# Kernel tuning notes

Measured on AMD Instinct MI355X. Metric: run time of the kernel, lower is better.

## Reference

```python
import jax, jax.numpy as jnp
import numpy as np

B, S, E, H, W, HID, V, OUT, L = 2, 2048, 512, 8, 5, 2048, 32000, 6, 6
DH = E // H
SCALE = DH ** -0.5
PAD = (W - 1) // 2
SK = S - W + 1  # number of k/v windows from torch unfold


def setup_inputs() -> dict:
    key = jax.random.key(0)
    ks = jax.random.split(key, 16)
    def g(i, shape, s):
        return jax.random.normal(ks[i], shape, jnp.float32) * s
    return {
        "inputs": jax.random.randint(ks[0], (B, S), 0, V),
        "emb": g(1, (V, E), 0.02),
        "ln_w": jnp.ones((E,), jnp.float32),
        "ln_b": jnp.zeros((E,), jnp.float32),
        "q_w": g(2, (E, E), E ** -0.5), "q_b": jnp.zeros((E,), jnp.float32),
        "k_w": g(3, (E, E), E ** -0.5), "k_b": jnp.zeros((E,), jnp.float32),
        "v_w": g(4, (E, E), E ** -0.5), "v_b": jnp.zeros((E,), jnp.float32),
        "fc1_w": g(5, (E, HID), E ** -0.5), "fc1_b": jnp.zeros((HID,), jnp.float32),
        "fc2_w": g(6, (HID, E), HID ** -0.5), "fc2_b": jnp.zeros((E,), jnp.float32),
        "out_w": g(7, (E * S, OUT), (E * S) ** -0.5), "out_b": jnp.zeros((OUT,), jnp.float32),
    }


def _pos_encoding():
    pos = jnp.arange(S, dtype=jnp.float32)[:, None]
    div = jnp.exp(jnp.arange(0, E, 2, dtype=jnp.float32) * (-np.log(10000.0) / E))
    pe = jnp.zeros((S, E), jnp.float32)
    pe = pe.at[:, 0::2].set(jnp.sin(pos * div)).at[:, 1::2].set(jnp.cos(pos * div))
    return pe


def reference(inputs, emb, ln_w, ln_b, q_w, q_b, k_w, k_b, v_w, v_b,
              fc1_w, fc1_b, fc2_w, fc2_b, out_w, out_b):
    x = emb[inputs] + _pos_encoding()  # [B,S,E]

    def ln(t):
        m = t.mean(-1, keepdims=True)
        v_ = t.var(-1, keepdims=True)
        return (t - m) / jnp.sqrt(v_ + 1e-5) * ln_w + ln_b

    def attn(x):
        def heads(w, b):
            return (x @ w + b).reshape(B, S, H, DH).transpose(0, 2, 1, 3)  # [B,H,S,dh]
        q, k, v = heads(q_w, q_b), heads(k_w, k_b), heads(v_w, v_b)
        qp = jnp.pad(q, ((0, 0), (0, 0), (PAD, PAD), (0, 0)))  # [B,H,S+W-1,dh]
        # torch unfold -> windows [..., dh, W]; einsum contracts dh AND W, so flatten both.
        q_un = jnp.stack([qp[:, :, j:j + S, :] for j in range(W)], axis=-1).reshape(B, H, S, DH * W)
        k_un = jnp.stack([k[:, :, j:j + SK, :] for j in range(W)], axis=-1).reshape(B, H, SK, DH * W)
        scores = jnp.einsum('bhqf,bhkf->bhqk', q_un, k_un) * SCALE  # [B,H,S,SK]
        a = jax.nn.softmax(scores, axis=-1)
        # output einsum 'bnqk,bnkdh->bnqd' sums attn-weighted v over k AND window dim;
        # since attn is independent of window pos, presum v over the window.
        v_sum = sum(v[:, :, j:j + SK, :] for j in range(W))  # [B,H,SK,dh]
        o = jnp.einsum('bhqk,bhkd->bhqd', a, v_sum)
        return o.transpose(0, 2, 1, 3).reshape(B, S, E)

    for _ in range(L):
        x = ln(attn(x))
        x = (jax.nn.relu(x @ fc1_w + fc1_b) @ fc2_w + fc2_b) + x
        x = ln(x)
    return x.reshape(B, -1) @ out_w + out_b  # [B,OUT]
```

## Files before the change

### kernel.cpp

```cpp
#include <hip/hip_runtime.h>
#include <math.h>


namespace {
constexpr int kB   = 2;
constexpr int kS   = 2048;
constexpr int kE   = 512;
constexpr int kH   = 8;
constexpr int kDH  = 64;
constexpr int kSK  = 2044;
constexpr int kHID = 2048;
constexpr int kL   = 6;
constexpr float kScaleL2 = 0.125f * 1.44269504088896f;
constexpr int kTok = kB * kS;
constexpr int kNX  = kTok * kE;
constexpr int kQKV = 3 * kE;
constexpr int kSQ  = 72;
constexpr int kSV  = 136;
}

using f16x8   = __attribute__((ext_vector_type(8))) _Float16;
using floatx4 = __attribute__((ext_vector_type(4))) float;
using uint2v  = __attribute__((ext_vector_type(2))) unsigned int;
using uint4v  = __attribute__((ext_vector_type(4))) unsigned int;

static __device__ __forceinline__ unsigned short f2h(float f) {
  return __builtin_bit_cast(unsigned short, (_Float16)f);
}
static __device__ __forceinline__ float h2f(unsigned short u) {
  return (float)__builtin_bit_cast(_Float16, u);
}
static __device__ __forceinline__ unsigned int pk2h(float a, float b) {
  return __builtin_bit_cast(unsigned int, __builtin_amdgcn_cvt_pkrtz(a, b));
}
static __device__ __forceinline__ void gload_lds16(const unsigned short* g,
                                                   unsigned short* l) {
  __builtin_amdgcn_global_load_lds(
      (const __attribute__((address_space(1))) void*)g,
      (__attribute__((address_space(3))) void*)l, 16, 0, 0);
}
static __device__ __forceinline__ float red16(float x, bool hi) {
  const unsigned u = __builtin_bit_cast(unsigned, x);
  const uint2v r = __builtin_amdgcn_permlane16_swap(u, u, false, false);
  return __builtin_bit_cast(float, hi ? r[0] : r[1]);
}
static __device__ __forceinline__ float red32(float x, bool hi) {
  const unsigned u = __builtin_bit_cast(unsigned, x);
  const uint2v r = __builtin_amdgcn_permlane32_swap(u, u, false, false);
  return __builtin_bit_cast(float, hi ? r[0] : r[1]);
}

__global__ __launch_bounds__(256) void embed_kernel(const int* __restrict__ idx,
        const float* __restrict__ emb, unsigned short* __restrict__ X) {
  const int bs  = blockIdx.x;
  const int s   = bs & (kS - 1);
  const int tok = idx[bs];
  const int t   = threadIdx.x;
#pragma unroll
  for (int r = 0; r < 2; ++r) {
    const int e = t + 256 * r;
    const int i = e >> 1;
    const float dv  = __expf((float)(2 * i) * (-9.210340371976184f / (float)kE));
    const float ang = (float)s * dv;
    const float pe  = (e & 1) ? cosf(ang) : sinf(ang);
    X[bs * kE + e] = f2h(emb[tok * kE + e] + pe);
  }
}

__global__ __launch_bounds__(256) void tcast_kernel(const float* __restrict__ src,
        unsigned short* __restrict__ dst, int K, int N) {
  __shared__ float t[32][33];
  const int tid = threadIdx.x;
  const int tx = tid & 31, ty = tid >> 5;
  const int n0 = blockIdx.x * 32, k0 = blockIdx.y * 32;
#pragma unroll
  for (int p = 0; p < 4; ++p)
    t[ty + 8 * p][tx] = src[(size_t)(k0 + ty + 8 * p) * N + n0 + tx];
  __syncthreads();
#pragma unroll
  for (int p = 0; p < 4; ++p)
    dst[(size_t)(n0 + ty + 8 * p) * K + k0 + tx] = f2h(t[tx][ty + 8 * p]);
}

__global__ __launch_bounds__(256) void qkvb_kernel(const float* __restrict__ qb,
        const float* __restrict__ kb, const float* __restrict__ vb,
        float* __restrict__ dst) {
  const int i = blockIdx.x * 256 + threadIdx.x;
  dst[i] = (i < 512) ? qb[i] : ((i < 1024) ? kb[i - 512] : vb[i - 1024]);
}

template <int RELU, int RES>
__global__ __launch_bounds__(256) void mfma_gemm(const unsigned short* __restrict__ A,
        const unsigned short* __restrict__ Bt, const float* __restrict__ bias,
        const unsigned short* __restrict__ Rm, unsigned short* __restrict__ C,
        int M, int N, int K) {
  __shared__ __align__(16) unsigned short As[2][128 * 32];
  __shared__ __align__(16) unsigned short Bs[2][128 * 32];
  const int tid = threadIdx.x;
  const int m0 = blockIdx.y * 128, n0 = blockIdx.x * 128;
  const int wid = tid >> 6, lane = tid & 63;
  const int lm = lane & 15, quad = lane >> 4;
  const int wm = (wid & 1) * 64, wn = (wid >> 1) * 64;
  const int bn = tid >> 2, bk = (tid & 3) * 8;
  const int wslot = wid * 512;
#pragma unroll
  for (int p = 0; p < 2; ++p) {
    gload_lds16(&A[(size_t)(m0 + bn + 64 * p) * K + bk], &As[0][wslot + p * 2048]);
    gload_lds16(&Bt[(size_t)(n0 + bn + 64 * p) * K + bk], &Bs[0][wslot + p * 2048]);
  }
  __syncthreads();
  floatx4 acc[4][4] = {};
  for (int k0 = 0; k0 < K; k0 += 32) {
    const int cur = (k0 >> 5) & 1;
    const int kn = k0 + 32;
    if (kn < K) {
#pragma unroll
      for (int p = 0; p < 2; ++p) {
        gload_lds16(&A[(size_t)(m0 + bn + 64 * p) * K + kn + bk],
                    &As[cur ^ 1][wslot + p * 2048]);
        gload_lds16(&Bt[(size_t)(n0 + bn + 64 * p) * K + kn + bk],
                    &Bs[cur ^ 1][wslot + p * 2048]);
      }
    }
    f16x8 af[4], bf[4];
#pragma unroll
    for (int t = 0; t < 4; ++t) {
      af[t] = *(const f16x8*)&As[cur][(wm + t * 16 + lm) * 32 + quad * 8];
      bf[t] = *(const f16x8*)&Bs[cur][(wn + t * 16 + lm) * 32 + quad * 8];
    }
#pragma unroll
    for (int mt = 0; mt < 4; ++mt)
#pragma unroll
      for (int nt = 0; nt < 4; ++nt)
        acc[mt][nt] = __builtin_amdgcn_mfma_f32_16x16x32_f16(
            af[mt], bf[nt], acc[mt][nt], 0, 0, 0);
    __syncthreads();
  }
#pragma unroll
  for (int mt = 0; mt < 4; ++mt) {
#pragma unroll
    for (int nt = 0; nt < 4; ++nt) {
      const int n = n0 + wn + nt * 16 + lm;
      const float bv = bias[n];
#pragma unroll
      for (int r = 0; r < 4; ++r) {
        const int m = m0 + wm + mt * 16 + quad * 4 + r;
        float o = acc[mt][nt][r] + bv;
        if (RES) o += h2f(Rm[(size_t)m * N + n]);
        if (RELU) o = fmaxf(o, 0.f);
        C[(size_t)m * N + n] = f2h(o);
      }
    }
  }
}

__global__ __launch_bounds__(256) void vsumt_kernel(const unsigned short* __restrict__ QKVh,
        unsigned short* __restrict__ VsT) {
  const int t0 = blockIdx.x * 64;
  const int h = blockIdx.y, b = blockIdx.z;
  const int tid = threadIdx.x;
  __shared__ float Ls[68 * 65];
  for (int id = tid; id < 68 * 8; id += 256) {
    const int row = id >> 3, d8 = (id & 7) * 8;
    const int gt = t0 + row;
    float v[8];
    if (gt < kS) {
      const unsigned short* p =
          &QKVh[(size_t)(b * kS + gt) * kQKV + 2 * kE + h * kDH + d8];
      const ushort4 a = *(const ushort4*)p;
      const ushort4 c = *(const ushort4*)(p + 4);
      v[0] = h2f(a.x); v[1] = h2f(a.y); v[2] = h2f(a.z); v[3] = h2f(a.w);
      v[4] = h2f(c.x); v[5] = h2f(c.y); v[6] = h2f(c.z); v[7] = h2f(c.w);
    } else {
#pragma unroll
      for (int j = 0; j < 8; ++j) v[j] = 0.f;
    }
#pragma unroll
    for (int j = 0; j < 8; ++j) Ls[row * 65 + d8 + j] = v[j];
  }
  __syncthreads();
  const int t4 = (tid & 15) * 4;
#pragma unroll
  for (int c = 0; c < 4; ++c) {
    const int d = (tid >> 4) + 16 * c;
    ushort4 o;
    unsigned short* op = (unsigned short*)&o;
#pragma unroll
    for (int j = 0; j < 4; ++j) {
      const int tl = t4 + j;
      float s = Ls[(tl + 0) * 65 + d] + Ls[(tl + 1) * 65 + d]
              + Ls[(tl + 2) * 65 + d] + Ls[(tl + 3) * 65 + d]
              + Ls[(tl + 4) * 65 + d];
      if (t0 + tl >= kSK) s = 0.f;
      op[j] = f2h(s);
    }
    *(ushort4*)&VsT[((size_t)(b * kH + h) * kDH + d) * (size_t)kS + t0 + t4] = o;
  }
}

__global__ __launch_bounds__(512) void flash_kernel(const unsigned short* __restrict__ QKVh,
        const unsigned short* __restrict__ VsT, unsigned short* __restrict__ O) {
  const int tid = threadIdx.x;
  const int qt = blockIdx.x, h = blockIdx.y, b = blockIdx.z;
  const int q0 = qt * 64;
  const int wid = tid >> 6, lane = tid & 63;
  const int lm = lane & 15, quad = lane >> 4;
  const bool h16 = (lane & 16) != 0, h32 = (lane & 32) != 0;
  const int wq = wid >> 2, wt = wid & 3;
  const int bh = b * kH + h;

  __shared__ __align__(16) unsigned short Qs[68 * kSQ];
  __shared__ __align__(16) unsigned short Ks[132 * kSQ];
  __shared__ __align__(16) unsigned short Vt[64 * kSV];
  __shared__ float mM[64][4], lM[64][4];

  for (int id = tid; id < 68 * 16; id += 512) {
    const int row = id >> 4, c4 = (id & 15) * 4;
    const int gq = q0 - 2 + row;
    ushort4 v = make_ushort4(0, 0, 0, 0);
    if (gq >= 0 && gq < kS)
      v = *(const ushort4*)&QKVh[(size_t)(b * kS + gq) * kQKV + h * kDH + c4];
    *(ushort4*)&Qs[row * kSQ + c4] = v;
  }

  const int prow = tid >> 4;
  const int pc4 = (tid & 15) * 4, pc8 = (tid & 15) * 8;
  ushort4 kreg[5];
  uint4 vreg[2];
#define PREFETCH(T0)                                                          \
  {                                                                           \
    _Pragma("unroll")                                                         \
    for (int p = 0; p < 5; ++p) {                                             \
      const int row = prow + 32 * p;                                          \
      ushort4 v = make_ushort4(0, 0, 0, 0);                                   \
      if (row < 132) {                                                        \
        const int gk = (T0) + row;                                            \
        if (gk < kS)                                                          \
          v = *(const ushort4*)&QKVh[(size_t)(b * kS + gk) * kQKV + kE +      \
                                     h * kDH + pc4];                          \
      }                                                                       \
      kreg[p] = v;                                                            \
    }                                                                         \
    _Pragma("unroll")                                                         \
    for (int p = 0; p < 2; ++p)                                               \
      vreg[p] = *(const uint4*)&VsT[((size_t)bh * kDH + prow + 32 * p) *      \
                                    (size_t)kS + (T0) + pc8];                 \
  }
  PREFETCH(0)

  float mrow[2], lrow[2];
  mrow[0] = mrow[1] = -1e30f;
  lrow[0] = lrow[1] = 0.f;
  floatx4 Oacc[2][4] = {};
  const int asrc = (lane >> 2) & 12;

  for (int t0 = 0; t0 < kSK; t0 += 128) {
    __syncthreads();
#pragma unroll
    for (int p = 0; p < 5; ++p) {
      const int row = prow + 32 * p;
      if (row < 132) *(ushort4*)&Ks[row * kSQ + pc4] = kreg[p];
    }
#pragma unroll
    for (int p = 0; p < 2; ++p)
      *(uint4*)&Vt[(prow + 32 * p) * kSV + pc8] = vreg[p];
    __syncthreads();
    const int tn = t0 + 128;
    if (tn < kSK) PREFETCH(tn)

    floatx4 sac[2][2] = {};
    __builtin_amdgcn_s_setprio(1);
#pragma unroll
    for (int kk = 0; kk < 10; ++kk) {
      const int w = kk >> 1, d0 = (kk & 1) * 32;
      const f16x8 kf0 = *(const f16x8*)&Ks[(wt * 32 + lm + w) * kSQ + d0 + quad * 8];
      const f16x8 kf1 = *(const f16x8*)&Ks[(wt * 32 + 16 + lm + w) * kSQ + d0 + quad * 8];
      const f16x8 qf0 = *(const f16x8*)&Qs[(wq * 32 + lm + w) * kSQ + d0 + quad * 8];
      const f16x8 qf1 = *(const f16x8*)&Qs[(wq * 32 + 16 + lm + w) * kSQ + d0 + quad * 8];
      sac[0][0] = __builtin_amdgcn_mfma_f32_16x16x32_f16(kf0, qf0, sac[0][0], 0, 0, 0);
      sac[0][1] = __builtin_amdgcn_mfma_f32_16x16x32_f16(kf0, qf1, sac[0][1], 0, 0, 0);
      sac[1][0] = __builtin_amdgcn_mfma_f32_16x16x32_f16(kf1, qf0, sac[1][0], 0, 0, 0);
      sac[1][1] = __builtin_amdgcn_mfma_f32_16x16x32_f16(kf1, qf1, sac[1][1], 0, 0, 0);
    }
    __builtin_amdgcn_s_setprio(0);

    if (t0 + wt * 32 + 32 > kSK) {
#pragma unroll
      for (int tf = 0; tf < 2; ++tf)
#pragma unroll
        for (int r = 0; r < 4; ++r) {
          const int tg = t0 + wt * 32 + tf * 16 + quad * 4 + r;
          if (tg >= kSK) { sac[tf][0][r] = -1e30f; sac[tf][1][r] = -1e30f; }
        }
    }

    float alpha_q[2];
    int skip_q[2];
    f16x8 pfrag[2];
#pragma unroll
    for (int qf = 0; qf < 2; ++qf) {
      float mx = fmaxf(
          fmaxf(fmaxf(sac[0][qf][0], sac[0][qf][1]), fmaxf(sac[0][qf][2], sac[0][qf][3])),
          fmaxf(fmaxf(sac[1][qf][0], sac[1][qf][1]), fmaxf(sac[1][qf][2], sac[1][qf][3])));
      mx = fmaxf(mx, red16(mx, h16));
      mx = fmaxf(mx, red32(mx, h32));
      const float mxs = mx * kScaleL2;
      const int skip = __all(mxs <= mrow[qf] + 8.f);
      float mnew, al;
      if (skip) { mnew = mrow[qf]; al = 1.f; }
      else      { mnew = fmaxf(mrow[qf], mxs); al = exp2f(mrow[qf] - mnew); }
      float e[2][4];
#pragma unroll
      for (int tf = 0; tf < 2; ++tf)
#pragma unroll
        for (int r = 0; r < 4; ++r)
          e[tf][r] = exp2f(fmaf(sac[tf][qf][r], kScaleL2, -mnew));
      float ps = ((e[0][0] + e[0][1]) + (e[0][2] + e[0][3]))
               + ((e[1][0] + e[1][1]) + (e[1][2] + e[1][3]));
      ps += red16(ps, h16);
      ps += red32(ps, h32);
      lrow[qf] = lrow[qf] * al + ps;
      mrow[qf] = mnew;
      alpha_q[qf] = al;
      skip_q[qf] = skip;
      const unsigned w00 = pk2h(e[0][0], e[0][1]);
      const unsigned w01 = pk2h(e[0][2], e[0][3]);
      const unsigned w10 = pk2h(e[1][0], e[1][1]);
      const unsigned w11 = pk2h(e[1][2], e[1][3]);
      const uint2v sA = __builtin_amdgcn_permlane32_swap(w00, w10, false, false);
      const uint2v dA = __builtin_amdgcn_permlane16_swap(sA[0], sA[1], false, false);
      const uint2v sB = __builtin_amdgcn_permlane32_swap(w01, w11, false, false);
      const uint2v dB = __builtin_amdgcn_permlane16_swap(sB[0], sB[1], false, false);
      uint4v fr;
      fr[0] = dA[0]; fr[1] = dB[0]; fr[2] = dA[1]; fr[3] = dB[1];
      pfrag[qf] = __builtin_bit_cast(f16x8, fr);
    }
    if (!(skip_q[0] && skip_q[1])) {
      float alpha_o[2][4];
#pragma unroll
      for (int qf = 0; qf < 2; ++qf)
#pragma unroll
        for (int r = 0; r < 4; ++r)
          alpha_o[qf][r] = __shfl(alpha_q[qf], asrc + r);
#pragma unroll
      for (int ms = 0; ms < 2; ++ms)
#pragma unroll
        for (int nt2 = 0; nt2 < 4; ++nt2)
#pragma unroll
          for (int r = 0; r < 4; ++r)
            Oacc[ms][nt2][r] *= alpha_o[ms][r];
    }
    {
      const int tcol = wt * 32 + quad * 8;
      __builtin_amdgcn_s_setprio(1);
#pragma unroll
      for (int nt2 = 0; nt2 < 4; ++nt2) {
        const f16x8 vf = *(const f16x8*)&Vt[(nt2 * 16 + lm) * kSV + tcol];
        Oacc[0][nt2] = __builtin_amdgcn_mfma_f32_16x16x32_f16(pfrag[0], vf, Oacc[0][nt2], 0, 0, 0);
        Oacc[1][nt2] = __builtin_amdgcn_mfma_f32_16x16x32_f16(pfrag[1], vf, Oacc[1][nt2], 0, 0, 0);
      }
      __builtin_amdgcn_s_setprio(0);
    }
  }
  if (quad == 0) {
#pragma unroll
    for (int qf = 0; qf < 2; ++qf) {
      const int row = wq * 32 + qf * 16 + lm;
      mM[row][wt] = mrow[qf];
      lM[row][wt] = lrow[qf];
    }
  }
  __syncthreads();
  float fac[2][4], invL[2][4];
#pragma unroll
  for (int qf = 0; qf < 2; ++qf)
#pragma unroll
    for (int r = 0; r < 4; ++r) {
      const int row = wq * 32 + qf * 16 + quad * 4 + r;
      const float M = fmaxf(fmaxf(mM[row][0], mM[row][1]),
                            fmaxf(mM[row][2], mM[row][3]));
      const float L = lM[row][0] * exp2f(mM[row][0] - M)
                    + lM[row][1] * exp2f(mM[row][1] - M)
                    + lM[row][2] * exp2f(mM[row][2] - M)
                    + lM[row][3] * exp2f(mM[row][3] - M);
      fac[qf][r] = exp2f(mM[row][wt] - M);
      invL[qf][r] = 1.f / L;
    }
  float* OfA = (float*)Vt;
  float* OfB = (float*)Ks;
  if (!(wt & 1)) {
    float* Of = (wt == 0) ? OfA : OfB;
#pragma unroll
    for (int ms = 0; ms < 2; ++ms)
#pragma unroll
      for (int nt2 = 0; nt2 < 4; ++nt2)
#pragma unroll
        for (int r = 0; r < 4; ++r)
          Of[(wq * 32 + ms * 16 + quad * 4 + r) * 68 + nt2 * 16 + lm] =
              Oacc[ms][nt2][r] * fac[ms][r];
  }
  __syncthreads();
  if (wt & 1) {
    float* Of = (wt == 1) ? OfA : OfB;
#pragma unroll
    for (int ms = 0; ms < 2; ++ms)
#pragma unroll
      for (int nt2 = 0; nt2 < 4; ++nt2)
#pragma unroll
        for (int r = 0; r < 4; ++r)
          Of[(wq * 32 + ms * 16 + quad * 4 + r) * 68 + nt2 * 16 + lm] +=
              Oacc[ms][nt2][r] * fac[ms][r];
  }
  __syncthreads();
  if (wt == 0) {
#pragma unroll
    for (int ms = 0; ms < 2; ++ms)
#pragma unroll
      for (int r = 0; r < 4; ++r) {
        const int row = wq * 32 + ms * 16 + quad * 4 + r;
        const int q = q0 + row;
#pragma unroll
        for (int nt2 = 0; nt2 < 4; ++nt2) {
          const float o = (OfA[row * 68 + nt2 * 16 + lm]
                           + OfB[row * 68 + nt2 * 16 + lm]) * invL[ms][r];
          O[(size_t)(b * kS + q) * kE + h * kDH + nt2 * 16 + lm] = f2h(o);
        }
      }
  }
}

__global__ __launch_bounds__(256) void ln_kernel(const unsigned short* __restrict__ Xin,
        const float* __restrict__ w, const float* __restrict__ bb,
        unsigned short* __restrict__ Y) {
  const int wid = threadIdx.x >> 6, lane = threadIdx.x & 63;
  const int row = blockIdx.x * 4 + wid;
  const unsigned short* xr = Xin + (size_t)row * kE + lane * 8;
  const ushort4 a = *(const ushort4*)xr;
  const ushort4 c = *(const ushort4*)(xr + 4);
  float v[8] = { h2f(a.x), h2f(a.y), h2f(a.z), h2f(a.w),
                 h2f(c.x), h2f(c.y), h2f(c.z), h2f(c.w) };
  float s = 0.f, sq = 0.f;
#pragma unroll
  for (int j = 0; j < 8; ++j) { s += v[j]; sq += v[j] * v[j]; }
#pragma unroll
  for (int off = 32; off; off >>= 1) {
    s  += __shfl_xor(s, off);
    sq += __shfl_xor(sq, off);
  }
  const float mean = s * (1.f / kE);
  const float var  = sq * (1.f / kE) - mean * mean;
  const float rstd = rsqrtf(var + 1e-5f);
  const float4 w0 = *(const float4*)&w[lane * 8];
  const float4 w1 = *(const float4*)&w[lane * 8 + 4];
  const float4 b0 = *(const float4*)&bb[lane * 8];
  const float4 b1 = *(const float4*)&bb[lane * 8 + 4];
  const float wa[8] = { w0.x, w0.y, w0.z, w0.w, w1.x, w1.y, w1.z, w1.w };
  const float ba[8] = { b0.x, b0.y, b0.z, b0.w, b1.x, b1.y, b1.z, b1.w };
  ushort4 o0, o1;
  unsigned short* op = (unsigned short*)&o0;
#pragma unroll
  for (int j = 0; j < 4; ++j) op[j] = f2h((v[j] - mean) * rstd * wa[j] + ba[j]);
  op = (unsigned short*)&o1;
#pragma unroll
  for (int j = 0; j < 4; ++j) op[j] = f2h((v[4 + j] - mean) * rstd * wa[4 + j] + ba[4 + j]);
  unsigned short* yr = Y + (size_t)row * kE + lane * 8;
  *(ushort4*)yr = o0;
  *(ushort4*)(yr + 4) = o1;
}

__global__ __launch_bounds__(256) void final_kernel(const unsigned short* __restrict__ X,
        const float* __restrict__ Wt, const float* __restrict__ bias,
        float* __restrict__ out) {
  const int b = blockIdx.y, chunk = blockIdx.x;
  const int tid = threadIdx.x;
  const unsigned short* xb = X + (size_t)b * (kS * kE);
  float acc[6] = {};
  const int k0 = chunk * 8192;
#pragma unroll 4
  for (int i = 0; i < 32; ++i) {
    const int kk = k0 + tid + i * 256;
    const float xv = h2f(xb[kk]);
    const float* wr = Wt + (size_t)kk * 6;
#pragma unroll
    for (int o = 0; o < 6; ++o) acc[o] = fmaf(xv, wr[o], acc[o]);
  }
#pragma unroll
  for (int o = 0; o < 6; ++o)
    for (int off = 32; off; off >>= 1) acc[o] += __shfl_down(acc[o], off);
  __shared__ float part[4][6];
  const int wid = tid >> 6;
  if ((tid & 63) == 0) {
#pragma unroll
    for (int o = 0; o < 6; ++o) part[wid][o] = acc[o];
  }
  __syncthreads();
  if (tid < 6) {
    float s2 = part[0][tid] + part[1][tid] + part[2][tid] + part[3][tid];
    if (chunk == 0) s2 += bias[tid];
    atomicAdd(&out[b * 6 + tid], s2);
  }
}

extern "C" void kernel_launch(void* const* d_in, const int* in_sizes, int n_in,
                              void* d_out, int out_size, void* d_ws, size_t ws_size,
                              hipStream_t stream) {
  (void)in_sizes; (void)n_in; (void)ws_size;
  const int*   tok   = (const int*)d_in[0];
  const float* emb   = (const float*)d_in[1];
  const float* ln_w  = (const float*)d_in[2];
  const float* ln_b  = (const float*)d_in[3];
  const float* q_w   = (const float*)d_in[4];
  const float* q_b   = (const float*)d_in[5];
  const float* k_w   = (const float*)d_in[6];
  const float* k_b   = (const float*)d_in[7];
  const float* v_w   = (const float*)d_in[8];
  const float* v_b   = (const float*)d_in[9];
  const float* fc1_w = (const float*)d_in[10];
  const float* fc1_b = (const float*)d_in[11];
  const float* fc2_w = (const float*)d_in[12];
  const float* fc2_b = (const float*)d_in[13];
  const float* out_w = (const float*)d_in[14];
  const float* out_b = (const float*)d_in[15];

  float* ws = (float*)d_ws;
  unsigned short* x16 = (unsigned short*)ws;
  unsigned short* y16 = (unsigned short*)(ws + (size_t)kNX / 2);
  float* regA = ws + (size_t)kNX;
  unsigned short* qkvh = (unsigned short*)regA;
  unsigned short* hbuf = (unsigned short*)regA;
  unsigned short* wqkvT = (unsigned short*)(ws + (size_t)3 * kNX);
  unsigned short* fc1T  = wqkvT + (size_t)kQKV * kE;
  unsigned short* fc2T  = fc1T + (size_t)kHID * kE;
  float* qkvb = (float*)(fc2T + (size_t)kE * kHID);
  unsigned short* vsT = (unsigned short*)(qkvb + kQKV);

  tcast_kernel<<<dim3(16, 16), 256, 0, stream>>>(q_w, wqkvT, kE, kE);
  tcast_kernel<<<dim3(16, 16), 256, 0, stream>>>(k_w, wqkvT + (size_t)kE * kE, kE, kE);
  tcast_kernel<<<dim3(16, 16), 256, 0, stream>>>(v_w, wqkvT + (size_t)2 * kE * kE, kE, kE);
  tcast_kernel<<<dim3(64, 16), 256, 0, stream>>>(fc1_w, fc1T, kE, kHID);
  tcast_kernel<<<dim3(16, 64), 256, 0, stream>>>(fc2_w, fc2T, kHID, kE);
  qkvb_kernel<<<dim3(6), 256, 0, stream>>>(q_b, k_b, v_b, qkvb);

  embed_kernel<<<dim3(kTok), 256, 0, stream>>>(tok, emb, x16);
  for (int l = 0; l < kL; ++l) {
    mfma_gemm<0, 0><<<dim3(kQKV / 128, kTok / 128), 256, 0, stream>>>(
        x16, wqkvT, qkvb, nullptr, qkvh, kTok, kQKV, kE);
    vsumt_kernel<<<dim3(kS / 64, kH, kB), 256, 0, stream>>>(qkvh, vsT);
    flash_kernel<<<dim3(kS / 64, kH, kB), 512, 0, stream>>>(qkvh, vsT, y16);
    ln_kernel<<<dim3(kTok / 4), 256, 0, stream>>>(y16, ln_w, ln_b, x16);
    mfma_gemm<1, 0><<<dim3(kHID / 128, kTok / 128), 256, 0, stream>>>(
        x16, fc1T, fc1_b, nullptr, hbuf, kTok, kHID, kE);
    mfma_gemm<0, 1><<<dim3(kE / 128, kTok / 128), 256, 0, stream>>>(
        hbuf, fc2T, fc2_b, x16, y16, kTok, kE, kHID);
    ln_kernel<<<dim3(kTok / 4), 256, 0, stream>>>(y16, ln_w, ln_b, x16);
  }
  hipMemsetAsync(d_out, 0, (size_t)out_size * sizeof(float), stream);
  final_kernel<<<dim3(128, kB), 256, 0, stream>>>(x16, out_w, out_b, (float*)d_out);
}
```

Before: 1.187 ms.

## Use 64-row GEMM tiles for QKV/FC2 and cache Q fragments in registers

Adds a BM template parameter to the MFMA GEMM so the QKV and FC2 projections run with 64x128 tiles. This doubles the block count on the 256-CU part, where the 128x128 grid gives only 384 or 128 blocks. In the flash attention kernel, the first half of each Q fragment (d0=0) is loaded once into registers before the key loop instead of being reread from LDS every tile. The smaller tiles lower per-block arithmetic intensity, and the register-cached Q raises register pressure and may reduce occupancy.

```diff
diff --git a/kernel.cpp b/kernel.cpp
--- a/kernel.cpp
+++ b/kernel.cpp
@@ -89,49 +89,55 @@
   dst[i] = (i < 512) ? qb[i] : ((i < 1024) ? kb[i - 512] : vb[i - 1024]);
 }
 
-template <int RELU, int RES>
+template <int BM, int RELU, int RES>
 __global__ __launch_bounds__(256) void mfma_gemm(const unsigned short* __restrict__ A,
         const unsigned short* __restrict__ Bt, const float* __restrict__ bias,
         const unsigned short* __restrict__ Rm, unsigned short* __restrict__ C,
         int M, int N, int K) {
-  __shared__ __align__(16) unsigned short As[2][128 * 32];
+  constexpr int NT = (BM == 128) ? 4 : 2;
+  constexpr int AP = BM / 64;
+  __shared__ __align__(16) unsigned short As[2][BM * 32];
   __shared__ __align__(16) unsigned short Bs[2][128 * 32];
   const int tid = threadIdx.x;
-  const int m0 = blockIdx.y * 128, n0 = blockIdx.x * 128;
+  const int m0 = blockIdx.y * BM, n0 = blockIdx.x * 128;
   const int wid = tid >> 6, lane = tid & 63;
   const int lm = lane & 15, quad = lane >> 4;
-  const int wm = (wid & 1) * 64, wn = (wid >> 1) * 64;
+  const int wm = (BM == 128) ? (wid & 1) * 64 : 0;
+  const int wn = (BM == 128) ? (wid >> 1) * 64 : wid * 32;
   const int bn = tid >> 2, bk = (tid & 3) * 8;
   const int wslot = wid * 512;
 #pragma unroll
-  for (int p = 0; p < 2; ++p) {
-    gload_lds16(&A[(size_t)(m0 + bn + 64 * p) * K + bk], &As[0][wslot + p * 2048]);
-    gload_lds16(&Bt[(size_t)(n0 + bn + 64 * p) * K + bk], &Bs[0][wslot + p * 2048]);
-  }
-  __syncthreads();
-  floatx4 acc[4][4] = {};
+  for (int p = 0; p < AP; ++p)
+    gload_lds16(&A[(size_t)(m0 + bn + 64 * p) * K + bk], &As[0][p * 2048 + wslot]);
+#pragma unroll
+  for (int p = 0; p < 2; ++p)
+    gload_lds16(&Bt[(size_t)(n0 + bn + 64 * p) * K + bk], &Bs[0][p * 2048 + wslot]);
+  __syncthreads();
+  floatx4 acc[4][NT] = {};
   for (int k0 = 0; k0 < K; k0 += 32) {
     const int cur = (k0 >> 5) & 1;
     const int kn = k0 + 32;
     if (kn < K) {
 #pragma unroll
-      for (int p = 0; p < 2; ++p) {
+      for (int p = 0; p < AP; ++p)
         gload_lds16(&A[(size_t)(m0 + bn + 64 * p) * K + kn + bk],
-                    &As[cur ^ 1][wslot + p * 2048]);
+                    &As[cur ^ 1][p * 2048 + wslot]);
+#pragma unroll
+      for (int p = 0; p < 2; ++p)
         gload_lds16(&Bt[(size_t)(n0 + bn + 64 * p) * K + kn + bk],
-                    &Bs[cur ^ 1][wslot + p * 2048]);
-      }
-    }
-    f16x8 af[4], bf[4];
-#pragma unroll
-    for (int t = 0; t < 4; ++t) {
+                    &Bs[cur ^ 1][p * 2048 + wslot]);
+    }
+    f16x8 af[4], bf[NT];
+#pragma unroll
+    for (int t = 0; t < 4; ++t)
       af[t] = *(const f16x8*)&As[cur][(wm + t * 16 + lm) * 32 + quad * 8];
+#pragma unroll
+    for (int t = 0; t < NT; ++t)
       bf[t] = *(const f16x8*)&Bs[cur][(wn + t * 16 + lm) * 32 + quad * 8];
-    }
 #pragma unroll
     for (int mt = 0; mt < 4; ++mt)
 #pragma unroll
-      for (int nt = 0; nt < 4; ++nt)
+      for (int nt = 0; nt < NT; ++nt)
         acc[mt][nt] = __builtin_amdgcn_mfma_f32_16x16x32_f16(
             af[mt], bf[nt], acc[mt][nt], 0, 0, 0);
     __syncthreads();
@@ -139,7 +145,7 @@
 #pragma unroll
   for (int mt = 0; mt < 4; ++mt) {
 #pragma unroll
-    for (int nt = 0; nt < 4; ++nt) {
+    for (int nt = 0; nt < NT; ++nt) {
       const int n = n0 + wn + nt * 16 + lm;
       const float bv = bias[n];
 #pragma unroll
@@ -248,6 +254,14 @@
   }
   PREFETCH(0)
 
+  __syncthreads();
+  f16x8 qreg[2][5];
+#pragma unroll
+  for (int w = 0; w < 5; ++w) {
+    qreg[0][w] = *(const f16x8*)&Qs[(wq * 32 + lm + w) * kSQ + quad * 8];
+    qreg[1][w] = *(const f16x8*)&Qs[(wq * 32 + 16 + lm + w) * kSQ + quad * 8];
+  }
+
   float mrow[2], lrow[2];
   mrow[0] = mrow[1] = -1e30f;
   lrow[0] = lrow[1] = 0.f;
@@ -275,8 +289,14 @@
       const int w = kk >> 1, d0 = (kk & 1) * 32;
       const f16x8 kf0 = *(const f16x8*)&Ks[(wt * 32 + lm + w) * kSQ + d0 + quad * 8];
       const f16x8 kf1 = *(const f16x8*)&Ks[(wt * 32 + 16 + lm + w) * kSQ + d0 + quad * 8];
-      const f16x8 qf0 = *(const f16x8*)&Qs[(wq * 32 + lm + w) * kSQ + d0 + quad * 8];
-      const f16x8 qf1 = *(const f16x8*)&Qs[(wq * 32 + 16 + lm + w) * kSQ + d0 + quad * 8];
+      f16x8 qf0, qf1;
+      if ((kk & 1) == 0) {
+        qf0 = qreg[0][w];
+        qf1 = qreg[1][w];
+      } else {
+        qf0 = *(const f16x8*)&Qs[(wq * 32 + lm + w) * kSQ + 32 + quad * 8];
+        qf1 = *(const f16x8*)&Qs[(wq * 32 + 16 + lm + w) * kSQ + 32 + quad * 8];
+      }
       sac[0][0] = __builtin_amdgcn_mfma_f32_16x16x32_f16(kf0, qf0, sac[0][0], 0, 0, 0);
       sac[0][1] = __builtin_amdgcn_mfma_f32_16x16x32_f16(kf0, qf1, sac[0][1], 0, 0, 0);
       sac[1][0] = __builtin_amdgcn_mfma_f32_16x16x32_f16(kf1, qf0, sac[1][0], 0, 0, 0);
@@ -543,14 +563,14 @@
 
   embed_kernel<<<dim3(kTok), 256, 0, stream>>>(tok, emb, x16);
   for (int l = 0; l < kL; ++l) {
-    mfma_gemm<0, 0><<<dim3(kQKV / 128, kTok / 128), 256, 0, stream>>>(
+    mfma_gemm<64, 0, 0><<<dim3(kQKV / 128, kTok / 64), 256, 0, stream>>>(
         x16, wqkvT, qkvb, nullptr, qkvh, kTok, kQKV, kE);
     vsumt_kernel<<<dim3(kS / 64, kH, kB), 256, 0, stream>>>(qkvh, vsT);
     flash_kernel<<<dim3(kS / 64, kH, kB), 512, 0, stream>>>(qkvh, vsT, y16);
     ln_kernel<<<dim3(kTok / 4), 256, 0, stream>>>(y16, ln_w, ln_b, x16);
-    mfma_gemm<1, 0><<<dim3(kHID / 128, kTok / 128), 256, 0, stream>>>(
+    mfma_gemm<128, 1, 0><<<dim3(kHID / 128, kTok / 128), 256, 0, stream>>>(
         x16, fc1T, fc1_b, nullptr, hbuf, kTok, kHID, kE);
-    mfma_gemm<0, 1><<<dim3(kE / 128, kTok / 128), 256, 0, stream>>>(
+    mfma_gemm<64, 0, 1><<<dim3(kE / 128, kTok / 64), 256, 0, stream>>>(
         hbuf, fc2T, fc2_b, x16, y16, kTok, kE, kHID);
     ln_kernel<<<dim3(kTok / 4), 256, 0, stream>>>(y16, ln_w, ln_b, x16);
   }
```

After: 1.318 ms. 1.11x slower.
